# Kernel tuning notes

Hardware: AMD Instinct MI355X
Metric: run time of the kernel (lower is better)

Reference implementation:

```python
import jax, jax.numpy as jnp
import numpy as np

N_GRAPHS = 100
BN_EPS = 1e-5
L = 4


def batch_norm(x, gamma, beta):
    # torch BatchNorm1d in training mode: biased batch statistics over the node dim
    mu = jnp.mean(x, axis=0)
    var = jnp.var(x, axis=0)
    return gamma * (x - mu) * jax.lax.rsqrt(var + BN_EPS) + beta


def setup_inputs() -> dict:
    key = jax.random.key(0)
    ks = jax.random.split(key, 24)
    N, E, IN, H, C = 50000, 600000, 128, 128, 10
    s = 0.05
    inp = {
        "h": jax.random.normal(ks[0], (N, IN), jnp.float32),
        "snorm_n": jax.random.uniform(ks[1], (N, 1), jnp.float32),
        "edge_src": jax.random.randint(ks[2], (E,), 0, N, jnp.int32),
        "edge_dst": jax.random.randint(ks[3], (E,), 0, N, jnp.int32),
        "graph_ids": jnp.sort(jax.random.randint(ks[4], (N,), 0, N_GRAPHS, jnp.int32)),
        # embedding_h
        "emb_W": jax.random.normal(ks[5], (IN, H), jnp.float32) * s,
        "emb_b": jnp.zeros((H,), jnp.float32),
        # per-layer GIN params, stacked over L layers
        "eps": jnp.zeros((L,), jnp.float32),
        "W1": jax.random.normal(ks[6], (L, H, H), jnp.float32) * s,
        "b1": jnp.zeros((L, H), jnp.float32),
        "g1": jnp.ones((L, H), jnp.float32),   # MLP internal BN gamma
        "be1": jnp.zeros((L, H), jnp.float32),  # MLP internal BN beta
        "W2": jax.random.normal(ks[7], (L, H, H), jnp.float32) * s,
        "b2": jnp.zeros((L, H), jnp.float32),
        "ga": jnp.ones((L, H), jnp.float32),    # ApplyNodeFunc BN gamma
        "ba": jnp.zeros((L, H), jnp.float32),
        "gl": jnp.ones((L, H), jnp.float32),    # GINLayer node BN gamma
        "bl": jnp.zeros((L, H), jnp.float32),
        # linears_prediction (L+1 of them)
        "pred_W": jax.random.normal(ks[8], (L + 1, H, C), jnp.float32) * s,
        "pred_b": jnp.zeros((L + 1, C), jnp.float32),
    }
    return inp


def reference(h, snorm_n, edge_src, edge_dst, graph_ids, emb_W, emb_b, eps,
              W1, b1, g1, be1, W2, b2, ga, ba, gl, bl, pred_W, pred_b):
    N = h.shape[0]
    h = h @ emb_W + emb_b  # embedding_h
    hidden_rep = [h]
    for i in range(L):
        h_in = h
        # sum-aggregate neighbor features (irregular gather + scatter-add)
        neigh = jax.ops.segment_sum(h[edge_src], edge_dst, num_segments=N)
        z = (1.0 + eps[i]) * h + neigh
        # ApplyNodeFunc: MLP (lin->BN->relu->lin) then BN then relu
        z = jax.nn.relu(batch_norm(z @ W1[i] + b1[i], g1[i], be1[i]))
        z = z @ W2[i] + b2[i]
        z = jax.nn.relu(batch_norm(z, ga[i], ba[i]))
        z = z * snorm_n                      # graph_norm
        z = batch_norm(z, gl[i], bl[i])      # batch_norm
        z = jax.nn.relu(z)
        h = h_in + z                         # residual (dropout p=0)
        hidden_rep.append(h)
    score = jnp.zeros((N_GRAPHS, pred_W.shape[-1]), h.dtype)
    for i, hr in enumerate(hidden_rep):
        pooled = jax.ops.segment_sum(hr, graph_ids, num_segments=N_GRAPHS)
        score = score + pooled @ pred_W[i] + pred_b[i]
    return score
```

## Files before the change

kernel.cpp:

```cpp
#include <hip/hip_runtime.h>

#define HD __device__ __forceinline__

static constexpr int H = 128;
static constexpr int G = 100;
static constexpr int L = 4;
static constexpr int C = 10;
static constexpr int DEGCAP = 64;

typedef __attribute__((ext_vector_type(8))) short short8;
typedef __attribute__((ext_vector_type(4))) float f32x4;

HD float bf2f(unsigned int u16) {
    return __uint_as_float(u16 << 16);
}
HD unsigned int f2bf(float f) {
    unsigned int u = __float_as_uint(f);
    u += 0x7fffu + ((u >> 16) & 1u);
    return u >> 16;
}

__global__ __launch_bounds__(256) void wprep_kernel(const float* __restrict__ embW,
                                                    const float* __restrict__ W1,
                                                    const float* __restrict__ W2,
                                                    unsigned short* __restrict__ WT) {
    int mat = blockIdx.y;
    const float* src = (mat == 0) ? embW
                     : (mat <= L) ? W1 + (size_t)(mat - 1) * H * H
                                  : W2 + (size_t)(mat - 1 - L) * H * H;
    int t = blockIdx.x * 256 + threadIdx.x;
    int col = t >> 7, k = t & 127;
    WT[(size_t)mat * H * H + col * H + k] = (unsigned short)f2bf(src[(size_t)k * H + col]);
}

__global__ void fill_kernel(const int* __restrict__ src, const int* __restrict__ dst, int E,
                            int* __restrict__ cnt, int* __restrict__ esrc) {
    int e = blockIdx.x * blockDim.x + threadIdx.x;
    if (e < E) {
        int d = dst[e];
        int pos = atomicAdd(&cnt[d], 1) & (DEGCAP - 1);
        esrc[(size_t)d * DEGCAP + pos] = src[e];
    }
}

__global__ __launch_bounds__(256, 4) void aggemm_kernel(
    const unsigned short* __restrict__ Hb, const int* __restrict__ cnt,
    const int* __restrict__ esrc, const float* __restrict__ eps, int layer,
    const unsigned short* __restrict__ WT, const float* __restrict__ bias,
    unsigned short* __restrict__ outB, int N,
    float* __restrict__ sum_out, float* __restrict__ sq_out) {
    __shared__ unsigned short As[64 * 136];
    int tid = threadIdx.x;
    int w = tid >> 6, lane = tid & 63, q = lane >> 4, m = lane & 15;
    int row0 = blockIdx.x * 64;
    int colbase = w * 32;

    short8 bfrag[2][4];
#pragma unroll
    for (int nt = 0; nt < 2; ++nt) {
        const unsigned short* wc = WT + (size_t)(colbase + nt * 16 + m) * H;
#pragma unroll
        for (int kk = 0; kk < 4; ++kk)
            bfrag[nt][kk] = *(const short8*)&wc[kk * 32 + q * 8];
    }

    const unsigned int* H2 = (const unsigned int*)Hb;
    float e1 = 1.0f + eps[layer];
    for (int i = 0; i < 16; ++i) {
        int r = w * 16 + i;
        int node = row0 + r;
        unsigned int out = 0;
        if (node < N) {
            unsigned int hv = H2[(size_t)node * 64 + lane];
            float ax[8], ay[8];
            ax[0] = e1 * bf2f(hv & 0xffffu);
            ay[0] = e1 * bf2f(hv >> 16);
#pragma unroll
            for (int u = 1; u < 8; ++u) { ax[u] = 0.f; ay[u] = 0.f; }
            int deg = min(cnt[node], DEGCAP);
            const int* ep = esrc + (size_t)node * DEGCAP;
            int j = 0;
            for (; j + 7 < deg; j += 8) {
                unsigned int v[8];
#pragma unroll
                for (int u = 0; u < 8; ++u) v[u] = H2[(size_t)ep[j + u] * 64 + lane];
#pragma unroll
                for (int u = 0; u < 8; ++u) {
                    ax[u] += bf2f(v[u] & 0xffffu);
                    ay[u] += bf2f(v[u] >> 16);
                }
            }
            for (; j + 1 < deg; j += 2) {
                unsigned int v0 = H2[(size_t)ep[j] * 64 + lane];
                unsigned int v1 = H2[(size_t)ep[j + 1] * 64 + lane];
                ax[0] += bf2f(v0 & 0xffffu); ay[0] += bf2f(v0 >> 16);
                ax[1] += bf2f(v1 & 0xffffu); ay[1] += bf2f(v1 >> 16);
            }
            if (j < deg) {
                unsigned int v0 = H2[(size_t)ep[j] * 64 + lane];
                ax[0] += bf2f(v0 & 0xffffu); ay[0] += bf2f(v0 >> 16);
            }
            float axs = ((ax[0] + ax[1]) + (ax[2] + ax[3])) + ((ax[4] + ax[5]) + (ax[6] + ax[7]));
            float ays = ((ay[0] + ay[1]) + (ay[2] + ay[3])) + ((ay[4] + ay[5]) + (ay[6] + ay[7]));
            out = f2bf(axs) | (f2bf(ays) << 16);
        }
        *(unsigned int*)&As[r * 136 + lane * 2] = out;
    }
    __syncthreads();

    f32x4 acc[4][2];
#pragma unroll
    for (int mt = 0; mt < 4; ++mt)
#pragma unroll
        for (int nt = 0; nt < 2; ++nt) acc[mt][nt] = (f32x4){0.f, 0.f, 0.f, 0.f};
#pragma unroll
    for (int kk = 0; kk < 4; ++kk) {
        short8 af[4];
#pragma unroll
        for (int mt = 0; mt < 4; ++mt)
            af[mt] = *(const short8*)&As[(mt * 16 + m) * 136 + kk * 32 + q * 8];
#pragma unroll
        for (int mt = 0; mt < 4; ++mt)
#pragma unroll
            for (int nt = 0; nt < 2; ++nt)
                acc[mt][nt] = __builtin_amdgcn_mfma_f32_16x16x32_bf16(
                    af[mt], bfrag[nt][kk], acc[mt][nt], 0, 0, 0);
    }

    float bs2[2] = {bias[colbase + m], bias[colbase + 16 + m]};
    float s[2] = {0.f, 0.f}, qq[2] = {0.f, 0.f};
#pragma unroll
    for (int mt = 0; mt < 4; ++mt)
#pragma unroll
        for (int nt = 0; nt < 2; ++nt) {
            int gcol = colbase + nt * 16 + m;
#pragma unroll
            for (int rg = 0; rg < 4; ++rg) {
                int grow = row0 + mt * 16 + q * 4 + rg;
                float v = acc[mt][nt][rg] + bs2[nt];
                if (grow < N) {
                    outB[(size_t)grow * H + gcol] = (unsigned short)f2bf(v);
                    s[nt] += v;
                    qq[nt] += v * v;
                }
            }
        }
#pragma unroll
    for (int nt = 0; nt < 2; ++nt) {
        float sv = s[nt], qv = qq[nt];
        sv += __shfl_xor(sv, 16); sv += __shfl_xor(sv, 32);
        qv += __shfl_xor(qv, 16); qv += __shfl_xor(qv, 32);
        if (q == 0) {
            atomicAdd(&sum_out[colbase + nt * 16 + m], sv);
            atomicAdd(&sq_out[colbase + nt * 16 + m], qv);
        }
    }
}

template <bool ABF16, bool TRANS, bool STATS, bool POOLF>
__global__ __launch_bounds__(256, 4) void mgemm_kernel(
    const float* __restrict__ Af, const unsigned short* __restrict__ Ab,
    const unsigned short* __restrict__ WT, const float* __restrict__ bias,
    const float* __restrict__ sum_in, const float* __restrict__ sq_in,
    const float* __restrict__ gam, const float* __restrict__ bet, float invN,
    unsigned short* __restrict__ outB,
    int N, float* __restrict__ sum_out, float* __restrict__ sq_out,
    const int* __restrict__ gids, float* __restrict__ pool) {
    __shared__ unsigned short As[64 * 136];
    __shared__ float cas[H], ccs[H];
    int tid = threadIdx.x;
    int w = tid >> 6, lane = tid & 63, q = lane >> 4, m = lane & 15;
    int row0 = blockIdx.x * 64;
    int colbase = w * 32;

    short8 bfrag[2][4];
#pragma unroll
    for (int nt = 0; nt < 2; ++nt) {
        const unsigned short* wc = WT + (size_t)(colbase + nt * 16 + m) * H;
#pragma unroll
        for (int kk = 0; kk < 4; ++kk)
            bfrag[nt][kk] = *(const short8*)&wc[kk * 32 + q * 8];
    }

    if (TRANS) {
        if (tid < H) {
            float mu = sum_in[tid] * invN;
            float var = sq_in[tid] * invN - mu * mu;
            float inv = rsqrtf(var + 1e-5f);
            float a = gam[tid] * inv;
            cas[tid] = a;
            ccs[tid] = bet[tid] - mu * a;
        }
        __syncthreads();
    }

    {
        int cc = tid & 15, rg = tid >> 4;
        int c0 = cc * 8;
        float a8[8], b8[8];
        if (TRANS) {
#pragma unroll
            for (int j = 0; j < 8; ++j) { a8[j] = cas[c0 + j]; b8[j] = ccs[c0 + j]; }
        }
#pragma unroll
        for (int rr = 0; rr < 4; ++rr) {
            int r = rg * 4 + rr;
            int gr = row0 + r;
            uint4 o = {0u, 0u, 0u, 0u};
            if (ABF16 && !TRANS) {
                if (gr < N) o = *(const uint4*)&Ab[(size_t)gr * H + c0];
            } else {
                float v[8] = {0.f, 0.f, 0.f, 0.f, 0.f, 0.f, 0.f, 0.f};
                if (gr < N) {
                    if (ABF16) {
                        uint4 x = *(const uint4*)&Ab[(size_t)gr * H + c0];
                        v[0] = bf2f(x.x & 0xffffu); v[1] = bf2f(x.x >> 16);
                        v[2] = bf2f(x.y & 0xffffu); v[3] = bf2f(x.y >> 16);
                        v[4] = bf2f(x.z & 0xffffu); v[5] = bf2f(x.z >> 16);
                        v[6] = bf2f(x.w & 0xffffu); v[7] = bf2f(x.w >> 16);
                    } else {
                        float4 x0 = *(const float4*)&Af[(size_t)gr * H + c0];
                        float4 x1 = *(const float4*)&Af[(size_t)gr * H + c0 + 4];
                        v[0] = x0.x; v[1] = x0.y; v[2] = x0.z; v[3] = x0.w;
                        v[4] = x1.x; v[5] = x1.y; v[6] = x1.z; v[7] = x1.w;
                    }
                }
                if (TRANS) {
#pragma unroll
                    for (int j = 0; j < 8; ++j) v[j] = fmaxf(a8[j] * v[j] + b8[j], 0.f);
                }
                o.x = f2bf(v[0]) | (f2bf(v[1]) << 16);
                o.y = f2bf(v[2]) | (f2bf(v[3]) << 16);
                o.z = f2bf(v[4]) | (f2bf(v[5]) << 16);
                o.w = f2bf(v[6]) | (f2bf(v[7]) << 16);
            }
            *(uint4*)&As[r * 136 + c0] = o;
        }
    }
    __syncthreads();

    f32x4 acc[4][2];
#pragma unroll
    for (int mt = 0; mt < 4; ++mt)
#pragma unroll
        for (int nt = 0; nt < 2; ++nt) acc[mt][nt] = (f32x4){0.f, 0.f, 0.f, 0.f};
#pragma unroll
    for (int kk = 0; kk < 4; ++kk) {
        short8 af[4];
#pragma unroll
        for (int mt = 0; mt < 4; ++mt)
            af[mt] = *(const short8*)&As[(mt * 16 + m) * 136 + kk * 32 + q * 8];
#pragma unroll
        for (int mt = 0; mt < 4; ++mt)
#pragma unroll
            for (int nt = 0; nt < 2; ++nt)
                acc[mt][nt] = __builtin_amdgcn_mfma_f32_16x16x32_bf16(
                    af[mt], bfrag[nt][kk], acc[mt][nt], 0, 0, 0);
    }

    float bs2[2] = {bias[colbase + m], bias[colbase + 16 + m]};
    float s[2] = {0.f, 0.f}, qq[2] = {0.f, 0.f};
#pragma unroll
    for (int mt = 0; mt < 4; ++mt)
#pragma unroll
        for (int nt = 0; nt < 2; ++nt) {
            int gcol = colbase + nt * 16 + m;
#pragma unroll
            for (int rg = 0; rg < 4; ++rg) {
                int grow = row0 + mt * 16 + q * 4 + rg;
                float v = acc[mt][nt][rg] + bs2[nt];
                if (grow < N) {
                    outB[(size_t)grow * H + gcol] = (unsigned short)f2bf(v);
                    if (STATS || POOLF) {
                        s[nt] += v;
                        if (STATS) qq[nt] += v * v;
                    }
                }
            }
        }

    if (STATS) {
#pragma unroll
        for (int nt = 0; nt < 2; ++nt) {
            float sv = s[nt], qv = qq[nt];
            sv += __shfl_xor(sv, 16); sv += __shfl_xor(sv, 32);
            qv += __shfl_xor(qv, 16); qv += __shfl_xor(qv, 32);
            if (q == 0) {
                atomicAdd(&sum_out[colbase + nt * 16 + m], sv);
                atomicAdd(&sq_out[colbase + nt * 16 + m], qv);
            }
        }
    }

    if (POOLF) {
        int last = min(row0 + 63, N - 1);
        bool uni = (gids[row0] == gids[last]);
        if (uni) {
            int g = gids[row0];
#pragma unroll
            for (int nt = 0; nt < 2; ++nt) {
                float sv = s[nt];
                sv += __shfl_xor(sv, 16); sv += __shfl_xor(sv, 32);
                if (q == 0) atomicAdd(&pool[g * H + colbase + nt * 16 + m], sv);
            }
        } else {
#pragma unroll
            for (int mt = 0; mt < 4; ++mt)
#pragma unroll
                for (int nt = 0; nt < 2; ++nt)
#pragma unroll
                    for (int rg = 0; rg < 4; ++rg) {
                        int grow = row0 + mt * 16 + q * 4 + rg;
                        if (grow < N) {
                            float v = acc[mt][nt][rg] + bs2[nt];
                            atomicAdd(&pool[gids[grow] * H + colbase + nt * 16 + m], v);
                        }
                    }
        }
    }
}

__global__ __launch_bounds__(256) void statsv_kernel(const unsigned short* __restrict__ UB,
                                                     const float* __restrict__ snorm,
                                                     const float* __restrict__ sum2, const float* __restrict__ sq2,
                                                     const float* __restrict__ ga, const float* __restrict__ ba,
                                                     float invN, int N,
                                                     float* __restrict__ sum3, float* __restrict__ sq3) {
    __shared__ float cas[H], ccs[H];
    int t = threadIdx.x;
    if (t < H) {
        float m = sum2[t] * invN;
        float var = sq2[t] * invN - m * m;
        float inv = rsqrtf(var + 1e-5f);
        float a = ga[t] * inv;
        cas[t] = a;
        ccs[t] = ba[t] - m * a;
    }
    __syncthreads();
    int col2 = t & 63, part = t >> 6;
    int c0 = col2 * 2, c1 = c0 + 1;
    float a0 = cas[c0], b0 = ccs[c0], a1 = cas[c1], b1 = ccs[c1];
    float s0 = 0.f, q0 = 0.f, s1 = 0.f, q1 = 0.f;
    const unsigned int* U2 = (const unsigned int*)UB;
    for (int r = blockIdx.x * 4 + part; r < N; r += gridDim.x * 4) {
        float sn = snorm[r];
        unsigned int v = U2[(size_t)r * 64 + col2];
        float v0 = fmaxf(a0 * bf2f(v & 0xffffu) + b0, 0.f) * sn;
        float v1 = fmaxf(a1 * bf2f(v >> 16) + b1, 0.f) * sn;
        s0 += v0; q0 += v0 * v0;
        s1 += v1; q1 += v1 * v1;
    }
    __shared__ float S[4][H], Q[4][H];
    S[part][c0] = s0; S[part][c1] = s1;
    Q[part][c0] = q0; Q[part][c1] = q1;
    __syncthreads();
    if (t < H) {
        atomicAdd(&sum3[t], S[0][t] + S[1][t] + S[2][t] + S[3][t]);
        atomicAdd(&sq3[t], Q[0][t] + Q[1][t] + Q[2][t] + Q[3][t]);
    }
}

__global__ __launch_bounds__(256) void tail_kernel(unsigned short* __restrict__ Hb,
                                                   const unsigned short* __restrict__ UB,
                                                   const float* __restrict__ snorm,
                                                   const float* __restrict__ sum2, const float* __restrict__ sq2,
                                                   const float* __restrict__ ga, const float* __restrict__ ba,
                                                   const float* __restrict__ sum3, const float* __restrict__ sq3,
                                                   const float* __restrict__ gl, const float* __restrict__ bl,
                                                   float invN, const int* __restrict__ gids,
                                                   float* __restrict__ pool, int N) {
    __shared__ float ca2[H], cc2[H], ca3[H], cc3[H];
    __shared__ float PS[8][H];
    int t = threadIdx.x;
    if (t < H) {
        float m2 = sum2[t] * invN, v2 = sq2[t] * invN - m2 * m2;
        float i2 = rsqrtf(v2 + 1e-5f), a2 = ga[t] * i2;
        ca2[t] = a2; cc2[t] = ba[t] - m2 * a2;
        float m3 = sum3[t] * invN, v3 = sq3[t] * invN - m3 * m3;
        float i3 = rsqrtf(v3 + 1e-5f), a3 = gl[t] * i3;
        ca3[t] = a3; cc3[t] = bl[t] - m3 * a3;
    }
    __syncthreads();
    int row0 = blockIdx.x * 32;
    int col4 = t & 31, rowg = t >> 5;
    int c0 = col4 * 4;
    float A2[4], B2[4], A3[4], B3[4];
#pragma unroll
    for (int j = 0; j < 4; ++j) {
        A2[j] = ca2[c0 + j]; B2[j] = cc2[c0 + j];
        A3[j] = ca3[c0 + j]; B3[j] = cc3[c0 + j];
    }
    bool uni = (gids[row0] == gids[min(row0 + 31, N - 1)]);
    float p[4] = {0.f, 0.f, 0.f, 0.f};
    const uint2* U4 = (const uint2*)UB;
    uint2* H4 = (uint2*)Hb;
#pragma unroll
    for (int rr = 0; rr < 4; ++rr) {
        int r = row0 + rowg * 4 + rr;
        if (r < N) {
            float sn = snorm[r];
            uint2 uv = U4[(size_t)r * 32 + col4];
            uint2 hv = H4[(size_t)r * 32 + col4];
            float u[4] = {bf2f(uv.x & 0xffffu), bf2f(uv.x >> 16), bf2f(uv.y & 0xffffu), bf2f(uv.y >> 16)};
            float h[4] = {bf2f(hv.x & 0xffffu), bf2f(hv.x >> 16), bf2f(hv.y & 0xffffu), bf2f(hv.y >> 16)};
#pragma unroll
            for (int j = 0; j < 4; ++j) {
                float v = fmaxf(A2[j] * u[j] + B2[j], 0.f) * sn;
                h[j] += fmaxf(A3[j] * v + B3[j], 0.f);
            }
            uint2 hb;
            hb.x = f2bf(h[0]) | (f2bf(h[1]) << 16);
            hb.y = f2bf(h[2]) | (f2bf(h[3]) << 16);
            H4[(size_t)r * 32 + col4] = hb;
            if (uni) {
                p[0] += h[0]; p[1] += h[1]; p[2] += h[2]; p[3] += h[3];
            } else {
                int g = gids[r];
#pragma unroll
                for (int j = 0; j < 4; ++j) atomicAdd(&pool[g * H + c0 + j], h[j]);
            }
        }
    }
    if (uni) {
#pragma unroll
        for (int j = 0; j < 4; ++j) PS[rowg][c0 + j] = p[j];
        __syncthreads();
        if (t < H) {
            float s = PS[0][t] + PS[1][t] + PS[2][t] + PS[3][t] +
                      PS[4][t] + PS[5][t] + PS[6][t] + PS[7][t];
            atomicAdd(&pool[gids[row0] * H + t], s);
        }
    }
}

__global__ void final_kernel(const float* __restrict__ pool, const float* __restrict__ pw,
                             const float* __restrict__ pb, float* __restrict__ out) {
    int g = blockIdx.x, t = threadIdx.x;
    __shared__ float p[H];
    float acc = 0.f;
    for (int i = 0; i <= L; ++i) {
        p[t] = pool[(size_t)(i * G + g) * H + t];
        __syncthreads();
        if (t < C) {
            float s = 0.f;
            for (int f = 0; f < H; ++f) s += p[f] * pw[(size_t)(i * H + f) * C + t];
            acc += s + pb[i * C + t];
        }
        __syncthreads();
    }
    if (t < C) out[g * C + t] = acc;
}

extern "C" void kernel_launch(void* const* d_in, const int* in_sizes, int n_in,
                              void* d_out, int out_size, void* d_ws, size_t ws_size,
                              hipStream_t stream) {
    const float* h_in  = (const float*)d_in[0];
    const float* snorm = (const float*)d_in[1];
    const int* esrc_in = (const int*)d_in[2];
    const int* edst_in = (const int*)d_in[3];
    const int* gids    = (const int*)d_in[4];
    const float* embW = (const float*)d_in[5];
    const float* embB = (const float*)d_in[6];
    const float* eps  = (const float*)d_in[7];
    const float* W1   = (const float*)d_in[8];
    const float* b1   = (const float*)d_in[9];
    const float* g1   = (const float*)d_in[10];
    const float* be1  = (const float*)d_in[11];
    const float* W2   = (const float*)d_in[12];
    const float* b2   = (const float*)d_in[13];
    const float* ga   = (const float*)d_in[14];
    const float* ba   = (const float*)d_in[15];
    const float* gl   = (const float*)d_in[16];
    const float* bl   = (const float*)d_in[17];
    const float* predW = (const float*)d_in[18];
    const float* predB = (const float*)d_in[19];

    const int N = in_sizes[0] / H;
    const int E = in_sizes[2];
    const float invN = 1.0f / (float)N;

    float* ws = (float*)d_ws;
    float* POOL = ws;
    float* STATS = POOL + (size_t)(L + 1) * G * H;
    int* CNT = (int*)(STATS + (size_t)L * 6 * H);
    unsigned short* WT = (unsigned short*)(CNT + N);
    int* ESRC = (int*)(WT + (size_t)9 * H * H);
    unsigned short* Hb = (unsigned short*)(ESRC + (size_t)N * DEGCAP);
    unsigned short* TB = Hb + (size_t)N * H;
    unsigned short* UB = TB + (size_t)N * H;

    size_t zbytes = ((size_t)(L + 1) * G * H + (size_t)L * 6 * H + N) * 4;
    hipMemsetAsync(POOL, 0, zbytes, stream);

    wprep_kernel<<<dim3(64, 9), 256, 0, stream>>>(embW, W1, W2, WT);
    fill_kernel<<<(E + 255) / 256, 256, 0, stream>>>(esrc_in, edst_in, E, CNT, ESRC);

    int gblocks = (N + 63) / 64;
    mgemm_kernel<false, false, false, true><<<gblocks, 256, 0, stream>>>(
        h_in, nullptr, WT, embB, nullptr, nullptr, nullptr, nullptr, invN,
        Hb, N, nullptr, nullptr, gids, POOL);

    for (int i = 0; i < L; ++i) {
        float* S1 = STATS + (size_t)i * 6 * H;
        float* Q1 = S1 + H;
        float* S2 = Q1 + H;
        float* Q2 = S2 + H;
        float* S3 = Q2 + H;
        float* Q3 = S3 + H;
        aggemm_kernel<<<gblocks, 256, 0, stream>>>(
            Hb, CNT, ESRC, eps, i, WT + (size_t)(1 + i) * H * H, b1 + (size_t)i * H,
            TB, N, S1, Q1);
        mgemm_kernel<true, true, true, false><<<gblocks, 256, 0, stream>>>(
            nullptr, TB, WT + (size_t)(1 + L + i) * H * H, b2 + (size_t)i * H,
            S1, Q1, g1 + (size_t)i * H, be1 + (size_t)i * H, invN,
            UB, N, S2, Q2, nullptr, nullptr);
        statsv_kernel<<<256, 256, 0, stream>>>(UB, snorm, S2, Q2,
                                               ga + (size_t)i * H, ba + (size_t)i * H, invN, N, S3, Q3);
        tail_kernel<<<(N + 31) / 32, 256, 0, stream>>>(Hb, UB, snorm,
                                                       S2, Q2, ga + (size_t)i * H, ba + (size_t)i * H,
                                                       S3, Q3, gl + (size_t)i * H, bl + (size_t)i * H,
                                                       invN, gids, POOL + (size_t)(i + 1) * G * H, N);
    }
    final_kernel<<<G, H, 0, stream>>>(POOL, predW, predB, (float*)d_out);
}
```

Baseline: 741.3 us.

## Split aggregation from GEMM and pad neighbor lists with a zero row

The fused gather+GEMM kernel is replaced by a standalone aggregation kernel that handles one node per wavefront, followed by a separate GEMM launch. The node-feature buffer gets a leading zero row, and edge source indices are shifted by one. Neighbor lists are padded to multiples of 16 with zero-index entries, which come from memsetting the ESRC array, so every gather loop runs a fixed unroll of 16 with no remainder branches. This is meant to give more independent loads in flight and better occupancy for the latency-bound gather, at the cost of an extra intermediate buffer write/read and another kernel launch per layer, plus a larger memset.

New measurement: 698.1 us. 5.8% less time.

```diff
diff --git a/kernel.cpp b/kernel.cpp
--- a/kernel.cpp
+++ b/kernel.cpp
@@ -23,8 +23,11 @@
 __global__ __launch_bounds__(256) void wprep_kernel(const float* __restrict__ embW,
                                                     const float* __restrict__ W1,
                                                     const float* __restrict__ W2,
-                                                    unsigned short* __restrict__ WT) {
+                                                    unsigned short* __restrict__ WT,
+                                                    unsigned short* __restrict__ Hb) {
     int mat = blockIdx.y;
+    if (mat == 0 && blockIdx.x == 0 && threadIdx.x < 64)
+        ((unsigned int*)Hb)[threadIdx.x] = 0u;
     const float* src = (mat == 0) ? embW
                      : (mat <= L) ? W1 + (size_t)(mat - 1) * H * H
                                   : W2 + (size_t)(mat - 1 - L) * H * H;
@@ -39,125 +42,43 @@
     if (e < E) {
         int d = dst[e];
         int pos = atomicAdd(&cnt[d], 1) & (DEGCAP - 1);
-        esrc[(size_t)d * DEGCAP + pos] = src[e];
-    }
-}
-
-__global__ __launch_bounds__(256, 4) void aggemm_kernel(
-    const unsigned short* __restrict__ Hb, const int* __restrict__ cnt,
-    const int* __restrict__ esrc, const float* __restrict__ eps, int layer,
-    const unsigned short* __restrict__ WT, const float* __restrict__ bias,
-    unsigned short* __restrict__ outB, int N,
-    float* __restrict__ sum_out, float* __restrict__ sq_out) {
-    __shared__ unsigned short As[64 * 136];
-    int tid = threadIdx.x;
-    int w = tid >> 6, lane = tid & 63, q = lane >> 4, m = lane & 15;
-    int row0 = blockIdx.x * 64;
-    int colbase = w * 32;
-
-    short8 bfrag[2][4];
-#pragma unroll
-    for (int nt = 0; nt < 2; ++nt) {
-        const unsigned short* wc = WT + (size_t)(colbase + nt * 16 + m) * H;
-#pragma unroll
-        for (int kk = 0; kk < 4; ++kk)
-            bfrag[nt][kk] = *(const short8*)&wc[kk * 32 + q * 8];
-    }
-
-    const unsigned int* H2 = (const unsigned int*)Hb;
+        esrc[(size_t)d * DEGCAP + pos] = src[e] + 1;
+    }
+}
+
+__global__ __launch_bounds__(256) void agg_kernel(const unsigned short* __restrict__ HbZ,
+                                                  const int* __restrict__ cnt,
+                                                  const int* __restrict__ esrc,
+                                                  const float* __restrict__ eps, int layer,
+                                                  unsigned short* __restrict__ ZB, int N) {
+    int node = blockIdx.x * 4 + (threadIdx.x >> 6);
+    int lane = threadIdx.x & 63;
+    if (node >= N) return;
+    const unsigned int* H2 = (const unsigned int*)HbZ;
     float e1 = 1.0f + eps[layer];
-    for (int i = 0; i < 16; ++i) {
-        int r = w * 16 + i;
-        int node = row0 + r;
-        unsigned int out = 0;
-        if (node < N) {
-            unsigned int hv = H2[(size_t)node * 64 + lane];
-            float ax[8], ay[8];
-            ax[0] = e1 * bf2f(hv & 0xffffu);
-            ay[0] = e1 * bf2f(hv >> 16);
-#pragma unroll
-            for (int u = 1; u < 8; ++u) { ax[u] = 0.f; ay[u] = 0.f; }
-            int deg = min(cnt[node], DEGCAP);
-            const int* ep = esrc + (size_t)node * DEGCAP;
-            int j = 0;
-            for (; j + 7 < deg; j += 8) {
-                unsigned int v[8];
-#pragma unroll
-                for (int u = 0; u < 8; ++u) v[u] = H2[(size_t)ep[j + u] * 64 + lane];
-#pragma unroll
-                for (int u = 0; u < 8; ++u) {
-                    ax[u] += bf2f(v[u] & 0xffffu);
-                    ay[u] += bf2f(v[u] >> 16);
-                }
-            }
-            for (; j + 1 < deg; j += 2) {
-                unsigned int v0 = H2[(size_t)ep[j] * 64 + lane];
-                unsigned int v1 = H2[(size_t)ep[j + 1] * 64 + lane];
-                ax[0] += bf2f(v0 & 0xffffu); ay[0] += bf2f(v0 >> 16);
-                ax[1] += bf2f(v1 & 0xffffu); ay[1] += bf2f(v1 >> 16);
-            }
-            if (j < deg) {
-                unsigned int v0 = H2[(size_t)ep[j] * 64 + lane];
-                ax[0] += bf2f(v0 & 0xffffu); ay[0] += bf2f(v0 >> 16);
-            }
-            float axs = ((ax[0] + ax[1]) + (ax[2] + ax[3])) + ((ax[4] + ax[5]) + (ax[6] + ax[7]));
-            float ays = ((ay[0] + ay[1]) + (ay[2] + ay[3])) + ((ay[4] + ay[5]) + (ay[6] + ay[7]));
-            out = f2bf(axs) | (f2bf(ays) << 16);
-        }
-        *(unsigned int*)&As[r * 136 + lane * 2] = out;
-    }
-    __syncthreads();
-
-    f32x4 acc[4][2];
-#pragma unroll
-    for (int mt = 0; mt < 4; ++mt)
-#pragma unroll
-        for (int nt = 0; nt < 2; ++nt) acc[mt][nt] = (f32x4){0.f, 0.f, 0.f, 0.f};
-#pragma unroll
-    for (int kk = 0; kk < 4; ++kk) {
-        short8 af[4];
-#pragma unroll
-        for (int mt = 0; mt < 4; ++mt)
-            af[mt] = *(const short8*)&As[(mt * 16 + m) * 136 + kk * 32 + q * 8];
-#pragma unroll
-        for (int mt = 0; mt < 4; ++mt)
-#pragma unroll
-            for (int nt = 0; nt < 2; ++nt)
-                acc[mt][nt] = __builtin_amdgcn_mfma_f32_16x16x32_bf16(
-                    af[mt], bfrag[nt][kk], acc[mt][nt], 0, 0, 0);
-    }
-
-    float bs2[2] = {bias[colbase + m], bias[colbase + 16 + m]};
-    float s[2] = {0.f, 0.f}, qq[2] = {0.f, 0.f};
-#pragma unroll
-    for (int mt = 0; mt < 4; ++mt)
-#pragma unroll
-        for (int nt = 0; nt < 2; ++nt) {
-            int gcol = colbase + nt * 16 + m;
-#pragma unroll
-            for (int rg = 0; rg < 4; ++rg) {
-                int grow = row0 + mt * 16 + q * 4 + rg;
-                float v = acc[mt][nt][rg] + bs2[nt];
-                if (grow < N) {
-                    outB[(size_t)grow * H + gcol] = (unsigned short)f2bf(v);
-                    s[nt] += v;
-                    qq[nt] += v * v;
-                }
-            }
-        }
-#pragma unroll
-    for (int nt = 0; nt < 2; ++nt) {
-        float sv = s[nt], qv = qq[nt];
-        sv += __shfl_xor(sv, 16); sv += __shfl_xor(sv, 32);
-        qv += __shfl_xor(qv, 16); qv += __shfl_xor(qv, 32);
-        if (q == 0) {
-            atomicAdd(&sum_out[colbase + nt * 16 + m], sv);
-            atomicAdd(&sq_out[colbase + nt * 16 + m], qv);
-        }
-    }
-}
-
-template <bool ABF16, bool TRANS, bool STATS, bool POOLF>
+    unsigned int hv = H2[(size_t)(node + 1) * 64 + lane];
+    float ax = e1 * bf2f(hv & 0xffffu);
+    float ay = e1 * bf2f(hv >> 16);
+    int deg = min(cnt[node], DEGCAP);
+    int degPad = min((deg + 15) & ~15, DEGCAP);
+    const int* ep = esrc + (size_t)node * DEGCAP;
+    for (int j = 0; j < degPad; j += 16) {
+        unsigned int v[16];
+#pragma unroll
+        for (int u = 0; u < 16; ++u) v[u] = H2[(size_t)ep[j + u] * 64 + lane];
+        float sx[4] = {0.f, 0.f, 0.f, 0.f}, sy[4] = {0.f, 0.f, 0.f, 0.f};
+#pragma unroll
+        for (int u = 0; u < 16; ++u) {
+            sx[u & 3] += bf2f(v[u] & 0xffffu);
+            sy[u & 3] += bf2f(v[u] >> 16);
+        }
+        ax += (sx[0] + sx[1]) + (sx[2] + sx[3]);
+        ay += (sy[0] + sy[1]) + (sy[2] + sy[3]);
+    }
+    ((unsigned int*)ZB)[(size_t)node * 64 + lane] = f2bf(ax) | (f2bf(ay) << 16);
+}
+
+template <bool ABF16, bool TRANS, bool STATS, bool POOLF, bool HOFF>
 __global__ __launch_bounds__(256, 4) void mgemm_kernel(
     const float* __restrict__ Af, const unsigned short* __restrict__ Ab,
     const unsigned short* __restrict__ WT, const float* __restrict__ bias,
@@ -270,7 +191,7 @@
                 int grow = row0 + mt * 16 + q * 4 + rg;
                 float v = acc[mt][nt][rg] + bs2[nt];
                 if (grow < N) {
-                    outB[(size_t)grow * H + gcol] = (unsigned short)f2bf(v);
+                    outB[(size_t)(HOFF ? grow + 1 : grow) * H + gcol] = (unsigned short)f2bf(v);
                     if (STATS || POOLF) {
                         s[nt] += v;
                         if (STATS) qq[nt] += v * v;
@@ -360,7 +281,7 @@
     }
 }
 
-__global__ __launch_bounds__(256) void tail_kernel(unsigned short* __restrict__ Hb,
+__global__ __launch_bounds__(256) void tail_kernel(unsigned short* __restrict__ HbZ,
                                                    const unsigned short* __restrict__ UB,
                                                    const float* __restrict__ snorm,
                                                    const float* __restrict__ sum2, const float* __restrict__ sq2,
@@ -393,14 +314,14 @@
     bool uni = (gids[row0] == gids[min(row0 + 31, N - 1)]);
     float p[4] = {0.f, 0.f, 0.f, 0.f};
     const uint2* U4 = (const uint2*)UB;
-    uint2* H4 = (uint2*)Hb;
+    uint2* H4 = (uint2*)HbZ;
 #pragma unroll
     for (int rr = 0; rr < 4; ++rr) {
         int r = row0 + rowg * 4 + rr;
         if (r < N) {
             float sn = snorm[r];
             uint2 uv = U4[(size_t)r * 32 + col4];
-            uint2 hv = H4[(size_t)r * 32 + col4];
+            uint2 hv = H4[(size_t)(r + 1) * 32 + col4];
             float u[4] = {bf2f(uv.x & 0xffffu), bf2f(uv.x >> 16), bf2f(uv.y & 0xffffu), bf2f(uv.y >> 16)};
             float h[4] = {bf2f(hv.x & 0xffffu), bf2f(hv.x >> 16), bf2f(hv.y & 0xffffu), bf2f(hv.y >> 16)};
 #pragma unroll
@@ -411,7 +332,7 @@
             uint2 hb;
             hb.x = f2bf(h[0]) | (f2bf(h[1]) << 16);
             hb.y = f2bf(h[2]) | (f2bf(h[3]) << 16);
-            H4[(size_t)r * 32 + col4] = hb;
+            H4[(size_t)(r + 1) * 32 + col4] = hb;
             if (uni) {
                 p[0] += h[0]; p[1] += h[1]; p[2] += h[2]; p[3] += h[3];
             } else {
@@ -483,20 +404,21 @@
     float* POOL = ws;
     float* STATS = POOL + (size_t)(L + 1) * G * H;
     int* CNT = (int*)(STATS + (size_t)L * 6 * H);
-    unsigned short* WT = (unsigned short*)(CNT + N);
-    int* ESRC = (int*)(WT + (size_t)9 * H * H);
-    unsigned short* Hb = (unsigned short*)(ESRC + (size_t)N * DEGCAP);
-    unsigned short* TB = Hb + (size_t)N * H;
-    unsigned short* UB = TB + (size_t)N * H;
-
-    size_t zbytes = ((size_t)(L + 1) * G * H + (size_t)L * 6 * H + N) * 4;
+    int* ESRC = CNT + N;
+    unsigned short* WT = (unsigned short*)(ESRC + (size_t)N * DEGCAP);
+    unsigned short* Hb = WT + (size_t)9 * H * H;
+    unsigned short* ZB = Hb + (size_t)(N + 1) * H;
+    unsigned short* TB = ZB + (size_t)N * H;
+    unsigned short* UB = ZB;
+
+    size_t zbytes = ((size_t)(L + 1) * G * H + (size_t)L * 6 * H + N + (size_t)N * DEGCAP) * 4;
     hipMemsetAsync(POOL, 0, zbytes, stream);
 
-    wprep_kernel<<<dim3(64, 9), 256, 0, stream>>>(embW, W1, W2, WT);
+    wprep_kernel<<<dim3(64, 9), 256, 0, stream>>>(embW, W1, W2, WT, Hb);
     fill_kernel<<<(E + 255) / 256, 256, 0, stream>>>(esrc_in, edst_in, E, CNT, ESRC);
 
     int gblocks = (N + 63) / 64;
-    mgemm_kernel<false, false, false, true><<<gblocks, 256, 0, stream>>>(
+    mgemm_kernel<false, false, false, true, true><<<gblocks, 256, 0, stream>>>(
         h_in, nullptr, WT, embB, nullptr, nullptr, nullptr, nullptr, invN,
         Hb, N, nullptr, nullptr, gids, POOL);
 
@@ -507,10 +429,12 @@
         float* Q2 = S2 + H;
         float* S3 = Q2 + H;
         float* Q3 = S3 + H;
-        aggemm_kernel<<<gblocks, 256, 0, stream>>>(
-            Hb, CNT, ESRC, eps, i, WT + (size_t)(1 + i) * H * H, b1 + (size_t)i * H,
-            TB, N, S1, Q1);
-        mgemm_kernel<true, true, true, false><<<gblocks, 256, 0, stream>>>(
+        agg_kernel<<<(N + 3) / 4, 256, 0, stream>>>(Hb, CNT, ESRC, eps, i, ZB, N);
+        mgemm_kernel<true, false, true, false, false><<<gblocks, 256, 0, stream>>>(
+            nullptr, ZB, WT + (size_t)(1 + i) * H * H, b1 + (size_t)i * H,
+            nullptr, nullptr, nullptr, nullptr, invN,
+            TB, N, S1, Q1, nullptr, nullptr);
+        mgemm_kernel<true, true, true, false, false><<<gblocks, 256, 0, stream>>>(
             nullptr, TB, WT + (size_t)(1 + L + i) * H * H, b2 + (size_t)i * H,
             S1, Q1, g1 + (size_t)i * H, be1 + (size_t)i * H, invN,
             UB, N, S2, Q2, nullptr, nullptr);
```
